# Optimization experiments

Measured on AMD Instinct MI355X. Metric: run time of the kernel, lower is better.

## Reference

```python
import jax, jax.numpy as jnp
import numpy as np

B, N, C, H, NL, NH = 8, 1024, 256, 512, 3, 8


def setup_inputs() -> dict:
    key = jax.random.key(0)
    ks = jax.random.split(key, 16)
    g = lambda k, shape: jax.random.normal(k, shape, jnp.float32) * 0.02
    return dict(
        concept_features=jax.random.normal(ks[0], (B, N, C), jnp.float32),
        adjacency_matrix=jax.random.uniform(ks[1], (B, N, N), jnp.float32),
        edge_types=jax.random.randint(ks[2], (B, N, N), 0, 10),
        concept_mask=jnp.ones((B, N), bool),
        W_emb=g(ks[3], (H, C)), b_emb=jnp.zeros((H,), jnp.float32),
        W_in=g(ks[4], (NL, 3 * H, H)), b_in=jnp.zeros((NL, 3 * H), jnp.float32),
        W_out=g(ks[5], (NL, H, H)), b_out=jnp.zeros((NL, H), jnp.float32),
        W_conv=g(ks[6], (NL, H, H)), b_conv=jnp.zeros((NL, H), jnp.float32),
        W_cls=g(ks[7], (1, H)), b_cls=jnp.zeros((1,), jnp.float32),
        W_diff=g(ks[8], (5, H)), b_diff=jnp.zeros((5,), jnp.float32),
        W_pre=g(ks[9], (1, 2 * H)), b_pre=jnp.zeros((1,), jnp.float32),
        W_pool=g(ks[10], (H, H)), b_pool=jnp.zeros((H,), jnp.float32),
    )


def reference(concept_features, adjacency_matrix, edge_types, concept_mask,
              W_emb, b_emb, W_in, b_in, W_out, b_out, W_conv, b_conv,
              W_cls, b_cls, W_diff, b_diff, W_pre, b_pre, W_pool, b_pool):
    Bq, Nc, _ = concept_features.shape
    Hd = W_emb.shape[0]
    dh = Hd // NH

    def mha(x, Wi, bi, Wo, bo):
        # torch nn.MultiheadAttention with batch_first=False: the (B,N,H)
        # input is treated as (seq=B, batch=N, embed=H) -> attention over B.
        qkv = x @ Wi.T + bi                      # (B,N,3H)
        q, k, v = jnp.split(qkv, 3, axis=-1)
        rs = lambda t: t.reshape(Bq, Nc, NH, dh)
        q, k, v = rs(q), rs(k), rs(v)
        sc = jnp.einsum('inhd,jnhd->nhij', q, k) / jnp.sqrt(jnp.float32(dh))
        a = jax.nn.softmax(sc, axis=-1)          # (N,NH,B,B)
        o = jnp.einsum('nhij,jnhd->inhd', a, v).reshape(Bq, Nc, Hd)
        return o @ Wo.T + bo

    def ln(x):  # F.layer_norm, no affine
        m = x.mean(-1, keepdims=True)
        v = ((x - m) ** 2).mean(-1, keepdims=True)
        return (x - m) * jax.lax.rsqrt(v + 1e-5)

    x = concept_features @ W_emb.T + b_emb       # (B,N,H)
    for l in range(W_in.shape[0]):
        att = mha(x, W_in[l], b_in[l], W_out[l], b_out[l])
        conv = att @ W_conv[l].T + b_conv[l]
        agg = jnp.einsum('bij,bjh->bih', adjacency_matrix, conv)
        x = ln(x + agg)

    mastery = x @ W_cls.T + b_cls                # (B,N,1)
    diff = x @ W_diff.T + b_diff                 # (B,N,5)

    # O(N^2) pairwise loop -> bilinear decomposition:
    # score(i,j) = x_i @ W_pre[:, :H].T + x_j @ W_pre[:, H:].T + b
    h1 = (x @ W_pre[:, :Hd].T)[..., 0]           # (B,N)
    h2 = (x @ W_pre[:, Hd:].T)[..., 0]           # (B,N)
    pair = h1[:, :, None] + h2[:, None, :] + b_pre[0]  # (B,N,N)
    off = ~np.eye(Nc, dtype=bool).reshape(-1)    # static mask, i!=j row-major
    prereq = pair.reshape(Bq, Nc * Nc)[:, off][..., None]  # (B,N*(N-1),1)

    graph = x.mean(axis=1) @ W_pool.T + b_pool   # (B,H)
    return (x, mastery, diff, prereq, graph)
```

## Files before the change

### kernel.cpp

```cpp
#include <hip/hip_runtime.h>
#include <hip/hip_bf16.h>

typedef unsigned short ushort_t;
typedef __attribute__((ext_vector_type(4))) float floatx4;
typedef __attribute__((ext_vector_type(8))) __bf16 bf16x8;
typedef __attribute__((ext_vector_type(4))) unsigned short ushortx4;

static __device__ __forceinline__ float b2f(ushort_t u) {
  union { unsigned int i; float f; } v; v.i = ((unsigned int)u) << 16; return v.f;
}
static __device__ __forceinline__ ushort_t f2b(float f) {
  unsigned int x = __float_as_uint(f);
  unsigned int r = (x + 0x7fffu + ((x >> 16) & 1u)) >> 16;
  return (ushort_t)r;
}
static __device__ __forceinline__ void glds16(const ushort_t* g, ushort_t* l) {
  __builtin_amdgcn_global_load_lds(
      (const __attribute__((address_space(1))) unsigned int*)g,
      (__attribute__((address_space(3))) unsigned int*)l, 16, 0, 0);
}

template<int MODE, bool ASPLIT, bool SPLITK>
__global__ __launch_bounds__(256, 3) void gemm_bt(
    const void* __restrict__ Ap, const ushort_t* __restrict__ Bm,
    const float* __restrict__ bias,
    float* __restrict__ CoutF, float* __restrict__ CoutF2,
    ushort_t* __restrict__ CoutB, ushort_t* __restrict__ CoutB2,
    int M, int N, int K, long aBatch, long bBatch, long cBatch)
{
  __shared__ __align__(16) ushort_t As[128 * 64];
  __shared__ __align__(16) ushort_t Bs[128 * 64];

  const int tid  = threadIdx.x;
  const int wid  = tid >> 6;
  const int lane = tid & 63;
  const int quad = lane >> 4;
  const int l16  = lane & 15;
  const int m0 = blockIdx.y * 128;
  const int n0 = blockIdx.x * 128;
  const int z  = SPLITK ? (blockIdx.z >> 1) : blockIdx.z;
  const int kh = SPLITK ? (blockIdx.z & 1) : 0;
  const int kbeg = SPLITK ? kh * (K >> 1) : 0;
  const int kend = SPLITK ? kbeg + (K >> 1) : K;
  float*    outF = (SPLITK && kh) ? CoutF2 : CoutF;
  ushort_t* outB = (SPLITK && kh) ? CoutB2 : CoutB;

  const ushort_t* Ab = (const ushort_t*)Ap + (long)z * aBatch;
  const float*    Af = (const float*)Ap + (long)z * aBatch;
  Bm += (long)z * bBatch;

  const int wr = (wid >> 1) * 64;
  const int wc = (wid & 1) * 64;

  const int srow = tid >> 3, ssub = (tid & 7) * 8;
  const long abase = (long)(m0 + srow) * K + ssub;
  const long bbase = (long)(n0 + srow) * K + ssub;

  floatx4 acc[4][4];
#pragma unroll
  for (int i = 0; i < 4; ++i)
#pragma unroll
    for (int j = 0; j < 4; ++j) acc[i][j] = (floatx4){0.f, 0.f, 0.f, 0.f};

  for (int k0 = kbeg; k0 < kend; k0 += 64) {
    __syncthreads();
    if constexpr (ASPLIT) {
#pragma unroll
      for (int p = 0; p < 4; ++p)
        glds16(Ab + abase + 32 * p * (long)K + k0, &As[tid * 8 + p * 2048]);
    } else {
#pragma unroll
      for (int p = 0; p < 8; ++p) {
        int c = tid + p * 256;
        int row = c >> 4, sub = (c & 15) * 4;
        floatx4 va = *(const floatx4*)(Af + (long)(m0 + row) * K + k0 + sub);
        ushortx4 ah;
#pragma unroll
        for (int r = 0; r < 4; ++r) ah[r] = f2b(va[r]);
        *(ushortx4*)(&As[row * 64 + sub]) = ah;
      }
    }
#pragma unroll
    for (int p = 0; p < 4; ++p)
      glds16(Bm + bbase + 32 * p * (long)K + k0, &Bs[tid * 8 + p * 2048]);
    __syncthreads();

#pragma unroll
    for (int kk = 0; kk < 2; ++kk) {
      bf16x8 a[4], b[4];
#pragma unroll
      for (int i = 0; i < 4; ++i)
        a[i] = *(const bf16x8*)(&As[(wr + i * 16 + l16) * 64 + kk * 32 + quad * 8]);
#pragma unroll
      for (int j = 0; j < 4; ++j)
        b[j] = *(const bf16x8*)(&Bs[(wc + j * 16 + l16) * 64 + kk * 32 + quad * 8]);
#pragma unroll
      for (int i = 0; i < 4; ++i)
#pragma unroll
        for (int j = 0; j < 4; ++j)
          acc[i][j] = __builtin_amdgcn_mfma_f32_16x16x32_bf16(a[i], b[j], acc[i][j], 0, 0, 0);
    }
  }

#pragma unroll
  for (int j = 0; j < 4; ++j) {
    int col = n0 + wc + j * 16 + l16;
    float bv = (bias != nullptr) ? bias[col] : 0.f;
#pragma unroll
    for (int i = 0; i < 4; ++i) {
      int mbase = m0 + wr + i * 16 + quad * 4;
      if constexpr (MODE == 0) {
#pragma unroll
        for (int r = 0; r < 4; ++r)
          outF[(long)z * cBatch + (long)(mbase + r) * N + col] = acc[i][j][r] + bv;
      } else if constexpr (MODE == 1) {
#pragma unroll
        for (int r = 0; r < 4; ++r)
          outB[(long)z * cBatch + (long)(mbase + r) * N + col] = f2b(acc[i][j][r] + bv);
      } else {
        int b = mbase >> 10, jrow = mbase & 1023;
        ushortx4 pk;
#pragma unroll
        for (int r = 0; r < 4; ++r) pk[r] = f2b(acc[i][j][r] + bv);
        *(ushortx4*)(CoutB + ((long)b * N + col) * 1024 + jrow) = pk;
      }
    }
  }
}

__global__ __launch_bounds__(256) void prep_kernel(
    const float* __restrict__ Win,  ushort_t* __restrict__ Winb,
    const float* __restrict__ Wemb, ushort_t* __restrict__ Wembb,
    const float* __restrict__ Wconv, ushort_t* __restrict__ Wcb,
    const float* __restrict__ ADJ,  ushort_t* __restrict__ ADJb,
    float* __restrict__ xm)
{
  const int bid = blockIdx.x, tid = threadIdx.x;
  const float* src; ushort_t* dst; long i;
  if (bid < 1152)      { src = Win;   dst = Winb;  i = (long)bid * 256 + tid; }
  else if (bid < 1216) { src = Wemb;  dst = Wembb; i = (long)(bid - 1152) * 256 + tid; }
  else if (bid < 1600) { src = Wconv; dst = Wcb;   i = (long)(bid - 1216) * 256 + tid; }
  else if (bid < 5696) { src = ADJ;   dst = ADJb;  i = (long)(bid - 1600) * 256 + tid; }
  else { xm[(bid - 5696) * 256 + tid] = 0.f; return; }
  floatx4 a = ((const floatx4*)src)[2 * i];
  floatx4 b = ((const floatx4*)src)[2 * i + 1];
  ushortx4 ha, hb;
#pragma unroll
  for (int r = 0; r < 4; ++r) { ha[r] = f2b(a[r]); hb[r] = f2b(b[r]); }
  ((ushortx4*)dst)[2 * i] = ha; ((ushortx4*)dst)[2 * i + 1] = hb;
}

__global__ __launch_bounds__(256) void transpose_split_kernel(
    const float* __restrict__ W, ushort_t* __restrict__ T)
{
  __shared__ float tile[64][65];
  const int k0 = blockIdx.x * 64, j0 = blockIdx.y * 64;
  const long base = (long)blockIdx.z * 262144;
  const int tid = threadIdx.x;
#pragma unroll
  for (int p = 0; p < 16; ++p) {
    int idx = tid + p * 256;
    int jj = idx >> 6, kk = idx & 63;
    tile[jj][kk] = W[base + (long)(j0 + jj) * 512 + k0 + kk];
  }
  __syncthreads();
#pragma unroll
  for (int p = 0; p < 16; ++p) {
    int idx = tid + p * 256;
    int kk = idx >> 6, jj = idx & 63;
    T[base + (long)(k0 + kk) * 512 + j0 + jj] = f2b(tile[jj][kk]);
  }
}

__global__ __launch_bounds__(256) void bfuse_kernel(
    const float* __restrict__ Wconv, const float* __restrict__ bout,
    const float* __restrict__ bconv, float* __restrict__ bf)
{
  const int w = threadIdx.x >> 6, lane = threadIdx.x & 63;
  const int gi = blockIdx.x * 4 + w;
  const int l = gi >> 9, o = gi & 511;
  float p = 0.f;
#pragma unroll
  for (int k = 0; k < 8; ++k)
    p += Wconv[(long)l * 262144 + (long)o * 512 + lane + 64 * k] *
         bout[l * 512 + lane + 64 * k];
#pragma unroll
  for (int msk = 1; msk <= 32; msk <<= 1) p += __shfl_xor(p, msk);
  if (lane == 0) bf[gi] = p + bconv[l * 512 + o];
}

__global__ __launch_bounds__(256) void attn_kernel(
    const ushort_t* __restrict__ qkv, ushort_t* __restrict__ outp)
{
  __shared__ float qs[4][8][65], ks[4][8][65], vs[4][8][65];
  __shared__ float aw[4][64];
  const int w    = threadIdx.x >> 6;
  const int lane = threadIdx.x & 63;
  const int p = blockIdx.x * 4 + w;
  const int n = p >> 3, h = p & 7;

  const long base = (long)n * 1536 + h * 64;
#pragma unroll
  for (int i = 0; i < 8; ++i) {
    long off = base + (long)i * 1024 * 1536;
    qs[w][i][lane] = b2f(qkv[off + lane]);
    ks[w][i][lane] = b2f(qkv[off + 512 + lane]);
    vs[w][i][lane] = b2f(qkv[off + 1024 + lane]);
  }
  __syncthreads();

  const int i = lane >> 3, j = lane & 7;
  float s = 0.f;
#pragma unroll 8
  for (int d = 0; d < 64; ++d) s += qs[w][i][d] * ks[w][j][d];
  s *= 0.125f;

  float m = s;
  m = fmaxf(m, __shfl_xor(m, 1));
  m = fmaxf(m, __shfl_xor(m, 2));
  m = fmaxf(m, __shfl_xor(m, 4));
  float e = __expf(s - m);
  float sum = e;
  sum += __shfl_xor(sum, 1);
  sum += __shfl_xor(sum, 2);
  sum += __shfl_xor(sum, 4);
  aw[w][lane] = e / sum;
  __syncthreads();

  const long ob = (long)n * 512 + h * 64 + lane;
#pragma unroll
  for (int ii = 0; ii < 8; ++ii) {
    float acc = 0.f;
#pragma unroll
    for (int jj = 0; jj < 8; ++jj) acc += aw[w][ii * 8 + jj] * vs[w][jj][lane];
    outp[ob + (long)ii * 1024 * 512] = f2b(acc);
  }
}

__global__ __launch_bounds__(256) void ln_kernel(
    const ushort_t* __restrict__ xb,
    const ushort_t* __restrict__ aggA, const ushort_t* __restrict__ aggB,
    ushort_t* __restrict__ outB)
{
  const int w = threadIdx.x >> 6, lane = threadIdx.x & 63;
  const long base = ((long)blockIdx.x * 4 + w) * 512;
  float v[8];
  float s = 0.f;
#pragma unroll
  for (int k = 0; k < 8; ++k) {
    long idx = base + lane + 64 * k;
    v[k] = b2f(xb[idx]) + b2f(aggA[idx]) + b2f(aggB[idx]);
    s += v[k];
  }
#pragma unroll
  for (int msk = 1; msk <= 32; msk <<= 1) s += __shfl_xor(s, msk);
  float mean = s * (1.f / 512.f);
  float vv = 0.f;
#pragma unroll
  for (int k = 0; k < 8; ++k) { float d = v[k] - mean; vv += d * d; }
#pragma unroll
  for (int msk = 1; msk <= 32; msk <<= 1) vv += __shfl_xor(vv, msk);
  float inv = rsqrtf(vv * (1.f / 512.f) + 1e-5f);
#pragma unroll
  for (int k = 0; k < 8; ++k)
    outB[base + lane + 64 * k] = f2b((v[base >= 0 ? k : k] - mean) * inv);
}

__global__ __launch_bounds__(256) void final_ln_heads_kernel(
    const ushort_t* __restrict__ xb,
    const ushort_t* __restrict__ aggA, const ushort_t* __restrict__ aggB,
    float* __restrict__ out_x,
    const float* __restrict__ Wcls, const float* __restrict__ bcls,
    const float* __restrict__ Wdiff, const float* __restrict__ bdiff,
    const float* __restrict__ Wpre,
    float* __restrict__ mastery, float* __restrict__ diff,
    float* __restrict__ h1, float* __restrict__ h2)
{
  const int w = threadIdx.x >> 6, lane = threadIdx.x & 63;
  const long row = (long)blockIdx.x * 4 + w;
  const long base = row * 512;
  float v[8];
  float s = 0.f;
#pragma unroll
  for (int k = 0; k < 8; ++k) {
    long idx = base + lane + 64 * k;
    v[k] = b2f(xb[idx]) + b2f(aggA[idx]) + b2f(aggB[idx]);
    s += v[k];
  }
#pragma unroll
  for (int msk = 1; msk <= 32; msk <<= 1) s += __shfl_xor(s, msk);
  float mean = s * (1.f / 512.f);
  float vv = 0.f;
#pragma unroll
  for (int k = 0; k < 8; ++k) { float d = v[k] - mean; vv += d * d; }
#pragma unroll
  for (int msk = 1; msk <= 32; msk <<= 1) vv += __shfl_xor(vv, msk);
  float inv = rsqrtf(vv * (1.f / 512.f) + 1e-5f);
#pragma unroll
  for (int k = 0; k < 8; ++k) {
    v[k] = (v[k] - mean) * inv;
    out_x[base + lane + 64 * k] = v[k];
  }
#pragma unroll
  for (int o = 0; o < 8; ++o) {
    const float* wp = (o == 0) ? Wcls
                    : (o <= 5) ? (Wdiff + (o - 1) * 512)
                    : (o == 6) ? Wpre : (Wpre + 512);
    float p = 0.f;
#pragma unroll
    for (int k = 0; k < 8; ++k) p += v[k] * wp[lane + 64 * k];
#pragma unroll
    for (int msk = 1; msk <= 32; msk <<= 1) p += __shfl_xor(p, msk);
    if (lane == 0) {
      if (o == 0)      mastery[row] = p + bcls[0];
      else if (o <= 5) diff[row * 5 + (o - 1)] = p + bdiff[o - 1];
      else if (o == 6) h1[row] = p;
      else             h2[row] = p;
    }
  }
}

__global__ __launch_bounds__(256) void prereq_kernel(
    const float* __restrict__ h1, const float* __restrict__ h2,
    const float* __restrict__ bpre, float* __restrict__ outp)
{
  const int b = blockIdx.y, i = blockIdx.x;
  const float base = h1[b * 1024 + i] + bpre[0];
  const long ob = (long)b * (1024 * 1023) + (long)i * 1023;
#pragma unroll
  for (int r = 0; r < 4; ++r) {
    int j = r * 256 + threadIdx.x;
    if (j == i) continue;
    int pos = (j < i) ? j : j - 1;
    outp[ob + pos] = base + h2[b * 1024 + j];
  }
}

__global__ __launch_bounds__(256) void pool_kernel(
    const float* __restrict__ x, float* __restrict__ xm)
{
  const int b = blockIdx.x >> 5, cc = (blockIdx.x >> 4) & 1, ns = blockIdx.x & 15;
  const int c = cc * 256 + threadIdx.x;
  float s = 0.f;
  for (int n = ns * 64; n < ns * 64 + 64; ++n)
    s += x[((long)b * 1024 + n) * 512 + c];
  atomicAdd(&xm[b * 512 + c], s);
}

__global__ __launch_bounds__(256) void graph_kernel(
    const float* __restrict__ xm, const float* __restrict__ Wpool,
    const float* __restrict__ bpool, float* __restrict__ g)
{
  const int gi = blockIdx.x * 256 + threadIdx.x;
  const int b = gi >> 9, o = gi & 511;
  float s = 0.f;
  for (int hh = 0; hh < 512; ++hh) s += xm[b * 512 + hh] * Wpool[o * 512 + hh];
  g[gi] = s * (1.f / 1024.f) + bpool[o];
}

extern "C" void kernel_launch(void* const* d_in, const int* in_sizes, int n_in,
                              void* d_out, int out_size, void* d_ws, size_t ws_size,
                              hipStream_t stream)
{
  const float* CF    = (const float*)d_in[0];
  const float* ADJ   = (const float*)d_in[1];
  const float* Wemb  = (const float*)d_in[4];
  const float* bemb  = (const float*)d_in[5];
  const float* Win   = (const float*)d_in[6];
  const float* bin   = (const float*)d_in[7];
  const float* Wout  = (const float*)d_in[8];
  const float* bout  = (const float*)d_in[9];
  const float* Wconv = (const float*)d_in[10];
  const float* bconv = (const float*)d_in[11];
  const float* Wcls  = (const float*)d_in[12];
  const float* bcls  = (const float*)d_in[13];
  const float* Wdiff = (const float*)d_in[14];
  const float* bdiff = (const float*)d_in[15];
  const float* Wpre  = (const float*)d_in[16];
  const float* bpre  = (const float*)d_in[17];
  const float* Wpool = (const float*)d_in[18];
  const float* bpool = (const float*)d_in[19];

  ushort_t* W = (ushort_t*)d_ws;
  ushort_t* xb   = W;
  ushort_t* qkvb = W + 4194304;
  ushort_t* cT    = qkvb;
  ushort_t* aggA  = qkvb + 4194304;
  ushort_t* aggB  = qkvb + 8388608;
  ushort_t* WoT   = qkvb + 4194304;
  ushort_t* Wembb = qkvb + 4980736;
  ushort_t* Wcb   = qkvb + 5111808;
  ushort_t* Winb = W + 16777216;
  ushort_t* Wfb  = W + 19136512;
  ushort_t* ADJb = W + 19922944;
  float* bfused = (float*)(W + 28311552);
  float* h1     = bfused + 1536;
  float* h2     = h1 + 8192;
  float* xm     = h2 + 8192;

  float* out_x       = (float*)d_out;
  float* out_mastery = out_x + 4194304;
  float* out_diff    = out_mastery + 8192;
  float* out_prereq  = out_diff + 40960;
  float* out_graph   = out_prereq + 8380416;
  ushort_t* aob = (ushort_t*)out_x;

  dim3 blk(256);

  prep_kernel<<<dim3(5712), blk, 0, stream>>>(Win, Winb, Wemb, Wembb,
                                              Wconv, Wcb, ADJ, ADJb, xm);
  transpose_split_kernel<<<dim3(8, 8, 3), blk, 0, stream>>>(Wout, WoT);
  gemm_bt<1, true, false><<<dim3(4, 4, 3), blk, 0, stream>>>(
      Wcb, WoT, nullptr, nullptr, nullptr, Wfb, nullptr,
      512, 512, 512, 262144, 262144, 262144);
  bfuse_kernel<<<dim3(384), blk, 0, stream>>>(Wconv, bout, bconv, bfused);

  gemm_bt<1, false, false><<<dim3(4, 64, 1), blk, 0, stream>>>(
      CF, Wembb, bemb, nullptr, nullptr, xb, nullptr, 8192, 512, 256, 0, 0, 0);

  for (int l = 0; l < 3; ++l) {
    gemm_bt<1, true, false><<<dim3(12, 64, 1), blk, 0, stream>>>(
        xb, Winb + (long)l * 786432, bin + l * 1536,
        nullptr, nullptr, qkvb, nullptr, 8192, 1536, 512, 0, 0, 0);
    attn_kernel<<<dim3(2048), blk, 0, stream>>>(qkvb, aob);
    gemm_bt<2, true, false><<<dim3(4, 64, 1), blk, 0, stream>>>(
        aob, Wfb + (long)l * 262144, bfused + l * 512,
        nullptr, nullptr, cT, nullptr, 8192, 512, 512, 0, 0, 0);
    gemm_bt<1, true, true><<<dim3(4, 8, 16), blk, 0, stream>>>(
        ADJb, cT, nullptr, nullptr, nullptr, aggA, aggB,
        1024, 512, 1024, 1048576, 524288, 524288);
    if (l < 2)
      ln_kernel<<<dim3(2048), blk, 0, stream>>>(xb, aggA, aggB, xb);
    else
      final_ln_heads_kernel<<<dim3(2048), blk, 0, stream>>>(
          xb, aggA, aggB, out_x, Wcls, bcls, Wdiff, bdiff, Wpre,
          out_mastery, out_diff, h1, h2);
  }

  prereq_kernel<<<dim3(1024, 8), blk, 0, stream>>>(h1, h2, bpre, out_prereq);
  pool_kernel<<<dim3(256), blk, 0, stream>>>(out_x, xm);
  graph_kernel<<<dim3(16), blk, 0, stream>>>(xm, Wpool, bpool, out_graph);
}
```

Before: 462.2 us.

## Vectorize attention loads per concept, remap GEMM tile order, merge prereq and pool kernels

The attention kernel now handles one concept per 512-thread block, with all 8 heads together, and loads the q/k/v rows for all 8 sequence positions using 16-byte vector loads into one shared buffer. This replaces scalar 2-byte loads and drops the second barrier, since each wave only reads its own attention weights. The GEMM block index is remapped so consecutive blocks walk down M first, which changes how tiles share cached B operands. The prereq and pool kernels are merged into a single launch to save one kernel launch. The larger shared buffer and block size may lower occupancy.

Result: no change. 457.9 us (-0.9%).

```diff
diff --git a/kernel.cpp b/kernel.cpp
--- a/kernel.cpp
+++ b/kernel.cpp
@@ -5,6 +5,7 @@
 typedef __attribute__((ext_vector_type(4))) float floatx4;
 typedef __attribute__((ext_vector_type(8))) __bf16 bf16x8;
 typedef __attribute__((ext_vector_type(4))) unsigned short ushortx4;
+typedef __attribute__((ext_vector_type(8))) unsigned short ushortx8;
 
 static __device__ __forceinline__ float b2f(ushort_t u) {
   union { unsigned int i; float f; } v; v.i = ((unsigned int)u) << 16; return v.f;
@@ -36,8 +37,9 @@
   const int lane = tid & 63;
   const int quad = lane >> 4;
   const int l16  = lane & 15;
-  const int m0 = blockIdx.y * 128;
-  const int n0 = blockIdx.x * 128;
+  const int lin = blockIdx.y * gridDim.x + blockIdx.x;
+  const int m0 = (lin % gridDim.y) * 128;
+  const int n0 = (lin / gridDim.y) * 128;
   const int z  = SPLITK ? (blockIdx.z >> 1) : blockIdx.z;
   const int kh = SPLITK ? (blockIdx.z & 1) : 0;
   const int kbeg = SPLITK ? kh * (K >> 1) : 0;
@@ -189,30 +191,33 @@
   if (lane == 0) bf[gi] = p + bconv[l * 512 + o];
 }
 
-__global__ __launch_bounds__(256) void attn_kernel(
+__global__ __launch_bounds__(512) void attn_kernel(
     const ushort_t* __restrict__ qkv, ushort_t* __restrict__ outp)
 {
-  __shared__ float qs[4][8][65], ks[4][8][65], vs[4][8][65];
-  __shared__ float aw[4][64];
-  const int w    = threadIdx.x >> 6;
-  const int lane = threadIdx.x & 63;
-  const int p = blockIdx.x * 4 + w;
-  const int n = p >> 3, h = p & 7;
-
-  const long base = (long)n * 1536 + h * 64;
-#pragma unroll
-  for (int i = 0; i < 8; ++i) {
-    long off = base + (long)i * 1024 * 1536;
-    qs[w][i][lane] = b2f(qkv[off + lane]);
-    ks[w][i][lane] = b2f(qkv[off + 512 + lane]);
-    vs[w][i][lane] = b2f(qkv[off + 1024 + lane]);
+  __shared__ float qs[8 * 1540];
+  __shared__ float aw[8][64];
+  const int tid = threadIdx.x;
+  const int n = blockIdx.x;
+
+  const ushort_t* src = qkv + (long)n * 1536;
+#pragma unroll
+  for (int p = 0; p < 3; ++p) {
+    int c = tid + p * 512;
+    int i = c / 192, off = (c % 192) * 8;
+    ushortx8 u = *(const ushortx8*)(src + (long)i * 1024 * 1536 + off);
+    float* d = &qs[i * 1540 + off];
+#pragma unroll
+    for (int r = 0; r < 8; ++r) d[r] = b2f(u[r]);
   }
   __syncthreads();
 
+  const int h    = tid >> 6;
+  const int lane = tid & 63;
   const int i = lane >> 3, j = lane & 7;
   float s = 0.f;
 #pragma unroll 8
-  for (int d = 0; d < 64; ++d) s += qs[w][i][d] * ks[w][j][d];
+  for (int d = 0; d < 64; ++d)
+    s += qs[i * 1540 + h * 64 + d] * qs[j * 1540 + 512 + h * 64 + d];
   s *= 0.125f;
 
   float m = s;
@@ -224,15 +229,15 @@
   sum += __shfl_xor(sum, 1);
   sum += __shfl_xor(sum, 2);
   sum += __shfl_xor(sum, 4);
-  aw[w][lane] = e / sum;
-  __syncthreads();
+  aw[h][lane] = e / sum;
 
   const long ob = (long)n * 512 + h * 64 + lane;
 #pragma unroll
   for (int ii = 0; ii < 8; ++ii) {
     float acc = 0.f;
 #pragma unroll
-    for (int jj = 0; jj < 8; ++jj) acc += aw[w][ii * 8 + jj] * vs[w][jj][lane];
+    for (int jj = 0; jj < 8; ++jj)
+      acc += aw[h][ii * 8 + jj] * qs[jj * 1540 + 1024 + h * 64 + lane];
     outp[ob + (long)ii * 1024 * 512] = f2b(acc);
   }
 }
@@ -263,7 +268,7 @@
   float inv = rsqrtf(vv * (1.f / 512.f) + 1e-5f);
 #pragma unroll
   for (int k = 0; k < 8; ++k)
-    outB[base + lane + 64 * k] = f2b((v[base >= 0 ? k : k] - mean) * inv);
+    outB[base + lane + 64 * k] = f2b((v[k] - mean) * inv);
 }
 
 __global__ __launch_bounds__(256) void final_ln_heads_kernel(
@@ -320,31 +325,32 @@
   }
 }
 
-__global__ __launch_bounds__(256) void prereq_kernel(
+__global__ __launch_bounds__(256) void epi_kernel(
     const float* __restrict__ h1, const float* __restrict__ h2,
-    const float* __restrict__ bpre, float* __restrict__ outp)
-{
-  const int b = blockIdx.y, i = blockIdx.x;
-  const float base = h1[b * 1024 + i] + bpre[0];
-  const long ob = (long)b * (1024 * 1023) + (long)i * 1023;
-#pragma unroll
-  for (int r = 0; r < 4; ++r) {
-    int j = r * 256 + threadIdx.x;
-    if (j == i) continue;
-    int pos = (j < i) ? j : j - 1;
-    outp[ob + pos] = base + h2[b * 1024 + j];
-  }
-}
-
-__global__ __launch_bounds__(256) void pool_kernel(
+    const float* __restrict__ bpre, float* __restrict__ outp,
     const float* __restrict__ x, float* __restrict__ xm)
 {
-  const int b = blockIdx.x >> 5, cc = (blockIdx.x >> 4) & 1, ns = blockIdx.x & 15;
-  const int c = cc * 256 + threadIdx.x;
-  float s = 0.f;
-  for (int n = ns * 64; n < ns * 64 + 64; ++n)
-    s += x[((long)b * 1024 + n) * 512 + c];
-  atomicAdd(&xm[b * 512 + c], s);
+  const int bid = blockIdx.x;
+  if (bid < 8192) {
+    const int b = bid >> 10, i = bid & 1023;
+    const float base = h1[b * 1024 + i] + bpre[0];
+    const long ob = (long)b * (1024 * 1023) + (long)i * 1023;
+#pragma unroll
+    for (int r = 0; r < 4; ++r) {
+      int j = r * 256 + threadIdx.x;
+      if (j == i) continue;
+      int pos = (j < i) ? j : j - 1;
+      outp[ob + pos] = base + h2[b * 1024 + j];
+    }
+  } else {
+    const int pb = bid - 8192;
+    const int b = pb >> 5, cc = (pb >> 4) & 1, ns = pb & 15;
+    const int c = cc * 256 + threadIdx.x;
+    float s = 0.f;
+    for (int n = ns * 64; n < ns * 64 + 64; ++n)
+      s += x[((long)b * 1024 + n) * 512 + c];
+    atomicAdd(&xm[b * 512 + c], s);
+  }
 }
 
 __global__ __launch_bounds__(256) void graph_kernel(
@@ -422,7 +428,7 @@
     gemm_bt<1, true, false><<<dim3(12, 64, 1), blk, 0, stream>>>(
         xb, Winb + (long)l * 786432, bin + l * 1536,
         nullptr, nullptr, qkvb, nullptr, 8192, 1536, 512, 0, 0, 0);
-    attn_kernel<<<dim3(2048), blk, 0, stream>>>(qkvb, aob);
+    attn_kernel<<<dim3(1024), dim3(512), 0, stream>>>(qkvb, aob);
     gemm_bt<2, true, false><<<dim3(4, 64, 1), blk, 0, stream>>>(
         aob, Wfb + (long)l * 262144, bfused + l * 512,
         nullptr, nullptr, cT, nullptr, 8192, 512, 512, 0, 0, 0);
@@ -437,7 +443,7 @@
           out_mastery, out_diff, h1, h2);
   }
 
-  prereq_kernel<<<dim3(1024, 8), blk, 0, stream>>>(h1, h2, bpre, out_prereq);
-  pool_kernel<<<dim3(256), blk, 0, stream>>>(out_x, xm);
+  epi_kernel<<<dim3(8448), blk, 0, stream>>>(h1, h2, bpre, out_prereq,
+                                             out_x, xm);
   graph_kernel<<<dim3(16), blk, 0, stream>>>(xm, Wpool, bpool, out_graph);
 }
```
